# Kernel tuning notes

Measured on AMD Instinct MI355X. Metric: run time of the kernel, lower is better.

The kernel has to match this reference:

```python
import jax, jax.numpy as jnp
import numpy as np

N = 200000
E = 3200000
EPS = 1e-5


def setup_inputs() -> dict:
    key = jax.random.key(0)
    ks = jax.random.split(key, 8)
    x = jax.random.normal(ks[0], (N, 128), dtype=jnp.float32)
    edge_index = jax.random.randint(ks[1], (2, E), 0, N, dtype=jnp.int32)
    def lin(k, fi, fo):
        s = 1.0 / np.sqrt(fi)
        return jax.random.uniform(k, (fi, fo), jnp.float32, -s, s)
    return {
        "x": x,
        "edge_index": edge_index,
        "W1": lin(ks[2], 128, 256), "b1": jnp.zeros((256,), jnp.float32),
        "gamma1": jnp.ones((256,), jnp.float32), "beta1": jnp.zeros((256,), jnp.float32),
        "W2": lin(ks[3], 256, 256), "b2": jnp.zeros((256,), jnp.float32),
        "gamma2": jnp.ones((256,), jnp.float32), "beta2": jnp.zeros((256,), jnp.float32),
        "W3": lin(ks[4], 256, 40), "b3": jnp.zeros((40,), jnp.float32),
    }


def _gcn_norm(edge_index):
    # add self-loops, compute symmetric GCN normalization
    loop = jnp.arange(N, dtype=jnp.int32)
    row = jnp.concatenate([edge_index[0], loop])
    col = jnp.concatenate([edge_index[1], loop])
    deg = jax.ops.segment_sum(jnp.ones_like(row, dtype=jnp.float32), row, num_segments=N)
    dinv = jax.lax.rsqrt(jnp.maximum(deg, 1.0))  # deg >= 1 due to self-loops
    norm = dinv[row] * dinv[col]  # [E+N]
    return row, col, norm


def _gcn_conv(x, W, b, row, col, norm):
    h = x @ W                                  # [N, Fout] small GEMM
    msg = h[col] * norm[:, None]               # gather + scale  [E+N, Fout]
    out = jax.ops.segment_sum(msg, row, num_segments=N)  # scatter-add
    return out + b


def _batchnorm(x, gamma, beta):
    mu = jnp.mean(x, axis=0)
    var = jnp.var(x, axis=0)
    return (x - mu) * jax.lax.rsqrt(var + EPS) * gamma + beta


def reference(x, edge_index, W1, b1, gamma1, beta1, W2, b2, gamma2, beta2, W3, b3):
    row, col, norm = _gcn_norm(edge_index)
    h = _gcn_conv(x, W1, b1, row, col, norm)
    h = jax.nn.relu(_batchnorm(h, gamma1, beta1))
    h = _gcn_conv(h, W2, b2, row, col, norm)
    h = jax.nn.relu(_batchnorm(h, gamma2, beta2))
    h = _gcn_conv(h, W3, b3, row, col, norm)
    return jax.nn.log_softmax(h, axis=-1)
```

## Files before the change

kernel.cpp:

```cpp
#include <hip/hip_runtime.h>
#include <hip/hip_bf16.h>

#define NNODES 200000
#define NEDGES 3200000
#define NBUCK 782
#define NEB 512
#define EPB (NEDGES / NEB)
#define CASTB 12500
#define EPS 1e-5f

typedef __bf16 bf16x8 __attribute__((ext_vector_type(8)));
typedef float  f32x4  __attribute__((ext_vector_type(4)));
typedef float  f32x2  __attribute__((ext_vector_type(2)));

__device__ __forceinline__ float bflo(unsigned u) { return __uint_as_float(u << 16); }
__device__ __forceinline__ float bfhi(unsigned u) { return __uint_as_float(u & 0xffff0000u); }
__device__ __forceinline__ unsigned short f2b(float f) {
    return __builtin_bit_cast(unsigned short, __float2bfloat16(f));
}
__device__ __forceinline__ unsigned pk2(float a, float b) {
    return (unsigned)f2b(a) | ((unsigned)f2b(b) << 16);
}
__device__ __forceinline__ unsigned bnrelu_pk(unsigned u, f32x2 c, f32x2 h) {
    f32x2 v = { __uint_as_float(u << 16), __uint_as_float(u & 0xffff0000u) };
    v = __builtin_elementwise_fma(v, c, h);
    const f32x2 z = {0.f, 0.f};
    v = __builtin_elementwise_max(v, z);
    return pk2(v[0], v[1]);
}

__global__ __launch_bounds__(256) void k_cnt(const int* __restrict__ row, int* __restrict__ cnt) {
    __shared__ int h[NBUCK];
    for (int i = threadIdx.x; i < NBUCK; i += 256) h[i] = 0;
    __syncthreads();
    const int e0 = blockIdx.x * EPB;
    for (int i = e0 + threadIdx.x; i < e0 + EPB; i += 256)
        atomicAdd(&h[row[i] >> 8], 1);
    __syncthreads();
    for (int i = threadIdx.x; i < NBUCK; i += 256)
        cnt[(size_t)blockIdx.x * NBUCK + i] = h[i];
}

__global__ __launch_bounds__(256) void k_bscan(int* __restrict__ cnt, int* __restrict__ btot) {
    const int wv = (blockIdx.x * 256 + threadIdx.x) >> 6;
    const int lane = threadIdx.x & 63;
    if (wv >= NBUCK) return;
    int v[8]; int s = 0;
#pragma unroll
    for (int j = 0; j < 8; ++j) {
        v[j] = cnt[(size_t)(lane * 8 + j) * NBUCK + wv];
        s += v[j];
    }
    int excl = s;
#pragma unroll
    for (int o = 1; o < 64; o <<= 1) {
        int t = __shfl_up(excl, o);
        if (lane >= o) excl += t;
    }
    excl -= s;
    if (lane == 63) btot[wv] = excl + s;
    int base = excl;
#pragma unroll
    for (int j = 0; j < 8; ++j) {
        int t = v[j];
        cnt[(size_t)(lane * 8 + j) * NBUCK + wv] = base;
        base += t;
    }
}

__global__ __launch_bounds__(1024) void k_btscan(const int* __restrict__ btot, int* __restrict__ bbase) {
    __shared__ int s[1024];
    int t = threadIdx.x;
    int v = (t < NBUCK) ? btot[t] : 0;
    s[t] = v;
    __syncthreads();
    for (int off = 1; off < 1024; off <<= 1) {
        int u = (t >= off) ? s[t - off] : 0;
        __syncthreads();
        s[t] += u;
        __syncthreads();
    }
    if (t < NBUCK) bbase[t + 1] = s[t];
    if (t == 0) bbase[0] = 0;
}

__global__ __launch_bounds__(256) void k_place(const int* __restrict__ row, const int* __restrict__ col,
                                               const int* __restrict__ cnt, const int* __restrict__ bbase,
                                               unsigned* __restrict__ ebuf) {
    __shared__ int base[NBUCK];
    for (int i = threadIdx.x; i < NBUCK; i += 256)
        base[i] = bbase[i] + cnt[(size_t)blockIdx.x * NBUCK + i];
    __syncthreads();
    const int e0 = blockIdx.x * EPB;
    for (int i = e0 + threadIdx.x; i < e0 + EPB; i += 256) {
        int r = row[i], c = col[i];
        int p = atomicAdd(&base[r >> 8], 1);
        ebuf[p] = ((unsigned)(r & 255) << 18) | (unsigned)c;
    }
}

__global__ __launch_bounds__(256) void k_sort2(const unsigned* __restrict__ ebuf,
                                               const int* __restrict__ bbase,
                                               int* __restrict__ offs, float* __restrict__ dinv,
                                               int* __restrict__ csr) {
    __shared__ int cnt[256];
    __shared__ int sofs[256];
    __shared__ int sc[256];
    const int b = blockIdx.x;
    const int t = threadIdx.x;
    const int n0 = b * 256;
    cnt[t] = 0;
    __syncthreads();
    const int s = bbase[b], e = bbase[b + 1];
    for (int i = s + t; i < e; i += 256)
        atomicAdd(&cnt[ebuf[i] >> 18], 1);
    __syncthreads();
    const int c = cnt[t];
    sc[t] = c;
    __syncthreads();
    for (int off = 1; off < 256; off <<= 1) {
        int v = (t >= off) ? sc[t - off] : 0;
        __syncthreads();
        sc[t] += v;
        __syncthreads();
    }
    const int excl = sc[t] - c;
    sofs[t] = s + excl;
    const int n = n0 + t;
    if (n < NNODES) {
        offs[n] = s + excl;
        dinv[n] = rsqrtf((float)(c + 1));
    }
    if (b == NBUCK - 1 && t == 0) offs[NNODES] = NEDGES;
    cnt[t] = 0;
    __syncthreads();
    for (int i = s + t; i < e; i += 256) {
        unsigned v = ebuf[i];
        int nl = v >> 18;
        int rank = atomicAdd(&cnt[nl], 1);
        csr[sofs[nl] + rank] = (int)(v & 0x3FFFFu);
    }
}

__device__ __forceinline__ void prepw_one(const float* __restrict__ W,
                                          unsigned short* __restrict__ Wswz,
                                          int K, int NOUT, int t) {
    int KSTEPS = K / 32;
    int lane = t & 63;
    int ks = (t >> 6) % KSTEPS;
    int g  = (t >> 6) / KSTEPS;
    int c = lane & 15, q = lane >> 4;
    int col = g * 16 + c;
    int k0 = ks * 32 + q * 8;
    unsigned short vals[8];
#pragma unroll
    for (int j = 0; j < 8; ++j)
        vals[j] = (col < NOUT) ? f2b(W[(size_t)(k0 + j) * NOUT + col]) : (unsigned short)0;
    *(uint4*)((char*)Wswz + (size_t)t * 16) = __builtin_bit_cast(uint4, vals);
}

__global__ __launch_bounds__(256) void k_prep(const float* __restrict__ x,
                                              const float* __restrict__ dinv,
                                              uint4* __restrict__ xb,
                                              const float* __restrict__ W1,
                                              const float* __restrict__ W2,
                                              const float* __restrict__ W3,
                                              unsigned short* __restrict__ w1s,
                                              unsigned short* __restrict__ w2s,
                                              unsigned short* __restrict__ w3s) {
    const int blk = blockIdx.x;
    if (blk < CASTB) {
        size_t t = (size_t)blk * 256 + threadIdx.x;
        int n = (int)(t >> 4);
        float d = dinv[n];
        const float4* xp = (const float4*)(x + t * 8);
        float4 a = xp[0], b = xp[1];
        uint4 o;
        o.x = pk2(a.x * d, a.y * d); o.y = pk2(a.z * d, a.w * d);
        o.z = pk2(b.x * d, b.y * d); o.w = pk2(b.z * d, b.w * d);
        xb[t] = o;
    } else {
        int t = (blk - CASTB) * 256 + threadIdx.x;
        if (t < 4096) prepw_one(W1, w1s, 128, 256, t);
        else if (t < 4096 + 8192) prepw_one(W2, w2s, 256, 256, t - 4096);
        else if (t < 4096 + 8192 + 1536) prepw_one(W3, w3s, 256, 40, t - 12288);
    }
}

__global__ __launch_bounds__(256) void k_aggf(const uint4* __restrict__ in,
                                              const int* __restrict__ offs,
                                              const int* __restrict__ csr,
                                              const float* __restrict__ dinv,
                                              uint4* __restrict__ out) {
    const int lane = threadIdx.x & 63;
    const int grp = lane >> 4;
    const int fl = lane & 15;
    const int node = blockIdx.x * 4 + (threadIdx.x >> 6);
    const int p0 = offs[node];
    const int K = offs[node + 1] - p0 + 1;
    float a0=0,a1=0,a2=0,a3=0,a4=0,a5=0,a6=0,a7=0;
    auto accum = [&](uint4 u) {
        a0 += bflo(u.x); a1 += bfhi(u.x);
        a2 += bflo(u.y); a3 += bfhi(u.y);
        a4 += bflo(u.z); a5 += bfhi(u.z);
        a6 += bflo(u.w); a7 += bfhi(u.w);
    };
    int k = 0;
    for (; k + 16 <= K; k += 16) {
        int j0 = k + grp;
        int i0 = (j0 == 0) ? node : csr[p0 + j0 - 1];
        int i1 = csr[p0 + k + 3 + grp];
        int i2 = csr[p0 + k + 7 + grp];
        int i3 = csr[p0 + k + 11 + grp];
        uint4 u0 = in[(size_t)i0 * 16 + fl];
        uint4 u1 = in[(size_t)i1 * 16 + fl];
        uint4 u2 = in[(size_t)i2 * 16 + fl];
        uint4 u3 = in[(size_t)i3 * 16 + fl];
        accum(u0); accum(u1); accum(u2); accum(u3);
    }
    for (; k + 8 <= K; k += 8) {
        int j0 = k + grp;
        int i0 = (j0 == 0) ? node : csr[p0 + j0 - 1];
        int i1 = csr[p0 + k + 3 + grp];
        uint4 u0 = in[(size_t)i0 * 16 + fl];
        uint4 u1 = in[(size_t)i1 * 16 + fl];
        accum(u0); accum(u1);
    }
    for (; k + 4 <= K; k += 4) {
        int j0 = k + grp;
        int i0 = (j0 == 0) ? node : csr[p0 + j0 - 1];
        accum(in[(size_t)i0 * 16 + fl]);
    }
    int rem = K - k;
    if (grp < rem) {
        int j0 = k + grp;
        int i0 = (j0 == 0) ? node : csr[p0 + j0 - 1];
        accum(in[(size_t)i0 * 16 + fl]);
    }
#define RED(v) v += __shfl_xor(v, 32); v += __shfl_xor(v, 16);
    RED(a0) RED(a1) RED(a2) RED(a3) RED(a4) RED(a5) RED(a6) RED(a7)
#undef RED
    if (grp == 0) {
        const float d = dinv[node];
        uint4 o;
        o.x = pk2(a0 * d, a1 * d); o.y = pk2(a2 * d, a3 * d);
        o.z = pk2(a4 * d, a5 * d); o.w = pk2(a6 * d, a7 * d);
        out[(size_t)node * 16 + fl] = o;
    }
}

__global__ __launch_bounds__(256) void k_aggb(const uint4* __restrict__ in,
                                              const int* __restrict__ offs,
                                              const int* __restrict__ csr,
                                              const float* __restrict__ dinv,
                                              uint4* __restrict__ out) {
    const int lane = threadIdx.x & 63;
    const int half = lane >> 5;
    const int fl = lane & 31;
    const int node = blockIdx.x * 4 + (threadIdx.x >> 6);
    const int p0 = offs[node];
    const int K = offs[node + 1] - p0 + 1;
    float a0=0,a1=0,a2=0,a3=0,a4=0,a5=0,a6=0,a7=0;
    auto accum = [&](uint4 u) {
        a0 += bflo(u.x); a1 += bfhi(u.x);
        a2 += bflo(u.y); a3 += bfhi(u.y);
        a4 += bflo(u.z); a5 += bfhi(u.z);
        a6 += bflo(u.w); a7 += bfhi(u.w);
    };
    auto idxAt = [&](int j) -> int { return (j == 0) ? node : csr[p0 + j - 1]; };
    int k = 0;
    for (; k + 16 <= K; k += 16) {
        int i0 = idxAt(k + half);
        int i1 = csr[p0 + k + 1 + half];
        int i2 = csr[p0 + k + 3 + half];
        int i3 = csr[p0 + k + 5 + half];
        int i4 = csr[p0 + k + 7 + half];
        int i5 = csr[p0 + k + 9 + half];
        int i6 = csr[p0 + k + 11 + half];
        int i7 = csr[p0 + k + 13 + half];
        uint4 u0 = in[(size_t)i0 * 32 + fl];
        uint4 u1 = in[(size_t)i1 * 32 + fl];
        uint4 u2 = in[(size_t)i2 * 32 + fl];
        uint4 u3 = in[(size_t)i3 * 32 + fl];
        uint4 u4 = in[(size_t)i4 * 32 + fl];
        uint4 u5 = in[(size_t)i5 * 32 + fl];
        uint4 u6 = in[(size_t)i6 * 32 + fl];
        uint4 u7 = in[(size_t)i7 * 32 + fl];
        accum(u0); accum(u1); accum(u2); accum(u3);
        accum(u4); accum(u5); accum(u6); accum(u7);
    }
    for (; k + 8 <= K; k += 8) {
        int i0 = idxAt(k + half);
        int i1 = csr[p0 + k + 1 + half];
        int i2 = csr[p0 + k + 3 + half];
        int i3 = csr[p0 + k + 5 + half];
        uint4 u0 = in[(size_t)i0 * 32 + fl];
        uint4 u1 = in[(size_t)i1 * 32 + fl];
        uint4 u2 = in[(size_t)i2 * 32 + fl];
        uint4 u3 = in[(size_t)i3 * 32 + fl];
        accum(u0); accum(u1); accum(u2); accum(u3);
    }
    for (; k + 2 <= K; k += 2) {
        accum(in[(size_t)idxAt(k + half) * 32 + fl]);
    }
    if (k < K && half == 0) {
        accum(in[(size_t)idxAt(k) * 32 + fl]);
    }
#define RED(v) v += __shfl_xor(v, 32);
    RED(a0) RED(a1) RED(a2) RED(a3) RED(a4) RED(a5) RED(a6) RED(a7)
#undef RED
    if (half == 0) {
        const float d = dinv[node];
        uint4 o;
        o.x = pk2(a0 * d, a1 * d); o.y = pk2(a2 * d, a3 * d);
        o.z = pk2(a4 * d, a5 * d); o.w = pk2(a6 * d, a7 * d);
        out[(size_t)node * 32 + fl] = o;
    }
}

__global__ __launch_bounds__(256) void k_agg3(const uint4* __restrict__ T3b,
                                              const int* __restrict__ offs,
                                              const int* __restrict__ csr,
                                              const float* __restrict__ dinv,
                                              const float* __restrict__ b3,
                                              float* __restrict__ out) {
    const int lane = threadIdx.x & 63;
    const int grp = lane / 5;
    const int fl = lane - grp * 5;
    const bool act = grp < 12;
    const int node = blockIdx.x * 4 + (threadIdx.x >> 6);
    const int p0 = offs[node];
    const int K = offs[node + 1] - p0 + 1;
    float a0=0,a1=0,a2=0,a3=0,a4=0,a5=0,a6=0,a7=0;
    auto accum = [&](uint4 u) {
        a0 += bflo(u.x); a1 += bfhi(u.x);
        a2 += bflo(u.y); a3 += bfhi(u.y);
        a4 += bflo(u.z); a5 += bfhi(u.z);
        a6 += bflo(u.w); a7 += bfhi(u.w);
    };
    const char* Tb = (const char*)T3b;
    int k = 0;
    if (act) {
        for (; k + 12 <= K; k += 12) {
            int j = k + grp;
            int i0 = (j == 0) ? node : csr[p0 + j - 1];
            accum(*(const uint4*)(Tb + (size_t)i0 * 128 + fl * 16));
        }
        int rem = K - k;
        if (grp < rem) {
            int j = k + grp;
            int i0 = (j == 0) ? node : csr[p0 + j - 1];
            accum(*(const uint4*)(Tb + (size_t)i0 * 128 + fl * 16));
        }
    }
#define RED3(v) { float t = __shfl(v, lane + 30); v += t; t = __shfl(v, lane + 15); v += t; \
                  float u1 = __shfl(v, lane + 5); float u2 = __shfl(v, lane + 10); v += u1 + u2; }
    RED3(a0) RED3(a1) RED3(a2) RED3(a3) RED3(a4) RED3(a5) RED3(a6) RED3(a7)
#undef RED3
    const float d = dinv[node];
    float v[8];
    if (grp == 0) {
        const float4* bp = (const float4*)(b3 + fl * 8);
        float4 b01 = bp[0], b23 = bp[1];
        v[0] = a0 * d + b01.x; v[1] = a1 * d + b01.y;
        v[2] = a2 * d + b01.z; v[3] = a3 * d + b01.w;
        v[4] = a4 * d + b23.x; v[5] = a5 * d + b23.y;
        v[6] = a6 * d + b23.z; v[7] = a7 * d + b23.w;
    } else {
#pragma unroll
        for (int j = 0; j < 8; ++j) v[j] = -INFINITY;
    }
    float m = v[0];
#pragma unroll
    for (int j = 1; j < 8; ++j) m = fmaxf(m, v[j]);
    float mm = __shfl(m, 0);
#pragma unroll
    for (int l = 1; l < 5; ++l) mm = fmaxf(mm, __shfl(m, l));
    float e = 0.f;
    if (grp == 0) {
#pragma unroll
        for (int j = 0; j < 8; ++j) e += __expf(v[j] - mm);
    }
    float s = __shfl(e, 0);
#pragma unroll
    for (int l = 1; l < 5; ++l) s += __shfl(e, l);
    float ls = __logf(s);
    if (grp == 0) {
        float* op = out + (size_t)node * 40 + fl * 8;
        float4 o0 = {v[0] - mm - ls, v[1] - mm - ls, v[2] - mm - ls, v[3] - mm - ls};
        float4 o1 = {v[4] - mm - ls, v[5] - mm - ls, v[6] - mm - ls, v[7] - mm - ls};
        *(float4*)op = o0;
        *(float4*)(op + 4) = o1;
    }
}

template <int K, int MW, int NW, int WNB, bool PRESCALE, bool BNA, bool STATS>
__global__ __launch_bounds__(MW * NW * 64) void k_gemm(const __hip_bfloat16* __restrict__ A,
                                                       const __hip_bfloat16* __restrict__ Wswz,
                                                       const float* __restrict__ dinvp,
                                                       const float* __restrict__ bnsc,
                                                       const float* __restrict__ bnsh,
                                                       unsigned short* __restrict__ Cout,
                                                       int M, int NOUT, int CS,
                                                       float* __restrict__ sums,
                                                       float* __restrict__ sq) {
    constexpr int KSTEPS = K / 32;
    const int lane = threadIdx.x & 63;
    const int wid  = threadIdx.x >> 6;
    const int wm = (wid % MW) * 64;
    const int wn = (wid / MW) * (WNB * 16);
    const long rowBase = (long)blockIdx.x * (MW * 64);
    const int cl = lane & 15, q = lane >> 4;

    const __hip_bfloat16* aptr[4];
#pragma unroll
    for (int mf = 0; mf < 4; ++mf) {
        long r = rowBase + wm + mf * 16 + cl;
        if (r > M - 1) r = M - 1;
        aptr[mf] = A + r * K + q * 8;
    }
    const __hip_bfloat16* bptr[WNB];
#pragma unroll
    for (int nf = 0; nf < WNB; ++nf) {
        int g = wn / 16 + nf;
        bptr[nf] = Wswz + (size_t)g * KSTEPS * 512 + (size_t)lane * 8;
    }

    f32x4 acc[4][WNB];
    const f32x4 z = {0.f, 0.f, 0.f, 0.f};
#pragma unroll
    for (int mf = 0; mf < 4; ++mf)
#pragma unroll
        for (int nf = 0; nf < WNB; ++nf) acc[mf][nf] = z;

#pragma unroll
    for (int ks = 0; ks < KSTEPS; ++ks) {
        f32x2 cp0, cp1, cp2, cp3, hp0, hp1, hp2, hp3;
        if constexpr (BNA) {
            const int k0 = ks * 32 + q * 8;
            const f32x2* cp = (const f32x2*)(bnsc + k0);
            const f32x2* hp = (const f32x2*)(bnsh + k0);
            cp0 = cp[0]; cp1 = cp[1]; cp2 = cp[2]; cp3 = cp[3];
            hp0 = hp[0]; hp1 = hp[1]; hp2 = hp[2]; hp3 = hp[3];
        }
        bf16x8 a[4], b[WNB];
#pragma unroll
        for (int mf = 0; mf < 4; ++mf) {
            uint4 u = *(const uint4*)(aptr[mf] + ks * 32);
            if constexpr (BNA) {
                uint4 o;
                o.x = bnrelu_pk(u.x, cp0, hp0);
                o.y = bnrelu_pk(u.y, cp1, hp1);
                o.z = bnrelu_pk(u.z, cp2, hp2);
                o.w = bnrelu_pk(u.w, cp3, hp3);
                u = o;
            }
            a[mf] = __builtin_bit_cast(bf16x8, u);
        }
#pragma unroll
        for (int nf = 0; nf < WNB; ++nf)
            b[nf] = __builtin_bit_cast(bf16x8, *(const uint4*)(bptr[nf] + ks * 512));
#pragma unroll
        for (int mf = 0; mf < 4; ++mf)
#pragma unroll
            for (int nf = 0; nf < WNB; ++nf)
                acc[mf][nf] = __builtin_amdgcn_mfma_f32_16x16x32_bf16(a[mf], b[nf], acc[mf][nf], 0, 0, 0);
    }

#pragma unroll
    for (int mf = 0; mf < 4; ++mf)
#pragma unroll
        for (int i = 0; i < 4; ++i) {
            long row = rowBase + wm + mf * 16 + q * 4 + i;
            if (row >= M) continue;
            float dv = PRESCALE ? dinvp[row] : 1.0f;
#pragma unroll
            for (int nf = 0; nf < WNB; ++nf) {
                int col = wn + nf * 16 + cl;
                if (col < NOUT)
                    Cout[row * CS + col] = f2b(PRESCALE ? acc[mf][nf][i] * dv : acc[mf][nf][i]);
            }
        }

    if constexpr (STATS) {
#pragma unroll
        for (int nf = 0; nf < WNB; ++nf) {
            float s = 0.f, s2 = 0.f;
#pragma unroll
            for (int mf = 0; mf < 4; ++mf)
#pragma unroll
                for (int i = 0; i < 4; ++i) {
                    long row = rowBase + wm + mf * 16 + q * 4 + i;
                    float v = (row < M) ? acc[mf][nf][i] : 0.f;
                    s += v; s2 += v * v;
                }
            s  += __shfl_xor(s, 16);  s  += __shfl_xor(s, 32);
            s2 += __shfl_xor(s2, 16); s2 += __shfl_xor(s2, 32);
            if (q == 0) {
                int col = wn + nf * 16 + cl;
                if (col < NOUT) {
                    atomicAdd(&sums[col], s);
                    atomicAdd(&sq[col], s2);
                }
            }
        }
    }
}

__global__ __launch_bounds__(256) void k_bnfin(const float* __restrict__ sums,
                                               const float* __restrict__ sq,
                                               const float* __restrict__ gamma,
                                               const float* __restrict__ beta,
                                               float* __restrict__ scale,
                                               float* __restrict__ shift) {
    const int t = threadIdx.x;
    float mu = sums[t] * (1.0f / NNODES);
    float var = sq[t] * (1.0f / NNODES) - mu * mu;
    if (var < 0.f) var = 0.f;
    float sc = gamma[t] * rsqrtf(var + EPS);
    scale[t] = sc;
    shift[t] = beta[t] - mu * sc;
}

__global__ __launch_bounds__(256) void k_stats(const uint4* __restrict__ Zu,
                                               float* __restrict__ sums, float* __restrict__ sq) {
    __shared__ float reds[8][256];
    __shared__ float redq[8][256];
    const int t = threadIdx.x;
    const int cg = t & 31;
    const int rs = t >> 5;
    const long r0 = (long)blockIdx.x * 256 + (long)rs * 32;
    float s[8], q[8];
#pragma unroll
    for (int j = 0; j < 8; ++j) { s[j] = 0.f; q[j] = 0.f; }
    for (int i = 0; i < 32; ++i) {
        long r = r0 + i;
        if (r >= NNODES) break;
        uint4 u = Zu[r * 32 + cg];
        float v0 = bflo(u.x), v1 = bfhi(u.x), v2 = bflo(u.y), v3 = bfhi(u.y);
        float v4 = bflo(u.z), v5 = bfhi(u.z), v6 = bflo(u.w), v7 = bfhi(u.w);
        s[0] += v0; q[0] += v0 * v0;  s[1] += v1; q[1] += v1 * v1;
        s[2] += v2; q[2] += v2 * v2;  s[3] += v3; q[3] += v3 * v3;
        s[4] += v4; q[4] += v4 * v4;  s[5] += v5; q[5] += v5 * v5;
        s[6] += v6; q[6] += v6 * v6;  s[7] += v7; q[7] += v7 * v7;
    }
#pragma unroll
    for (int j = 0; j < 8; ++j) {
        reds[rs][cg * 8 + j] = s[j];
        redq[rs][cg * 8 + j] = q[j];
    }
    __syncthreads();
    float S = 0.f, Q = 0.f;
#pragma unroll
    for (int j = 0; j < 8; ++j) { S += reds[j][t]; Q += redq[j][t]; }
    atomicAdd(&sums[t], S);
    atomicAdd(&sq[t], Q);
}

extern "C" void kernel_launch(void* const* d_in, const int* in_sizes, int n_in,
                              void* d_out, int out_size, void* d_ws, size_t ws_size,
                              hipStream_t stream) {
    const float* x   = (const float*)d_in[0];
    const int*   ei  = (const int*)d_in[1];
    const float* W1  = (const float*)d_in[2];
    const float* g1  = (const float*)d_in[4];
    const float* be1 = (const float*)d_in[5];
    const float* W2  = (const float*)d_in[6];
    const float* g2  = (const float*)d_in[8];
    const float* be2 = (const float*)d_in[9];
    const float* W3  = (const float*)d_in[10];
    const float* b3  = (const float*)d_in[11];

    char* w = (char*)d_ws;
    size_t o = 0;
    auto alloc = [&](size_t b) { size_t r = o; o += (b + 255) & ~(size_t)255; return r; };
    int*   offs = (int*)(w + alloc((size_t)(NNODES + 1) * 4));
    float* dinv = (float*)(w + alloc((size_t)NNODES * 4));
    int*   cnt  = (int*)(w + alloc((size_t)NEB * NBUCK * 4));
    int*   btot = (int*)(w + alloc(NBUCK * 4));
    int*   bbase= (int*)(w + alloc((NBUCK + 1) * 4));
    unsigned* ebuf = (unsigned*)(w + alloc((size_t)NEDGES * 4));
    int*   csr  = (int*)(w + alloc((size_t)NEDGES * 4));
    float* stats = (float*)(w + alloc(4 * 256 * 4 + 32));
    float* bnp   = (float*)(w + alloc(4 * 256 * 4));
    unsigned short* w1s = (unsigned short*)(w + alloc(65536));
    unsigned short* w2s = (unsigned short*)(w + alloc(131072));
    unsigned short* w3s = (unsigned short*)(w + alloc(24576));
    __hip_bfloat16* xb   = (__hip_bfloat16*)(w + alloc((size_t)NNODES * 128 * 2));
    __hip_bfloat16* buf0 = (__hip_bfloat16*)(w + alloc((size_t)NNODES * 128 * 2));
    __hip_bfloat16* buf1 = (__hip_bfloat16*)(w + alloc((size_t)NNODES * 256 * 2));
    __hip_bfloat16* buf2 = (__hip_bfloat16*)(w + alloc((size_t)NNODES * 256 * 2));

    float* sums1 = stats;       float* sq1 = stats + 256;
    float* sums2 = stats + 512; float* sq2 = stats + 768;
    float* scale1 = bnp;        float* shift1 = bnp + 256;
    float* scale2 = bnp + 512;  float* shift2 = bnp + 768;

    hipMemsetAsync(stats, 0, 4 * 256 * 4 + 32, stream);

    const int SB = (NNODES + 255) / 256;
    k_cnt<<<NEB, 256, 0, stream>>>(ei, cnt);
    k_bscan<<<(NBUCK * 64 + 255) / 256, 256, 0, stream>>>(cnt, btot);
    k_btscan<<<1, 1024, 0, stream>>>(btot, bbase);
    k_place<<<NEB, 256, 0, stream>>>(ei, ei + NEDGES, cnt, bbase, ebuf);
    k_sort2<<<NBUCK, 256, 0, stream>>>(ebuf, bbase, offs, dinv, csr);
    k_prep<<<CASTB + 54, 256, 0, stream>>>(x, dinv, (uint4*)xb, W1, W2, W3, w1s, w2s, w3s);

    const dim3 g64((NNODES + 63) / 64, 1);

    k_aggf<<<NNODES / 4, 256, 0, stream>>>((const uint4*)xb, offs, csr, dinv, (uint4*)buf0);
    k_gemm<128, 1, 4, 4, false, false, true><<<g64, 256, 0, stream>>>(buf0, (const __hip_bfloat16*)w1s, nullptr, nullptr, nullptr, (unsigned short*)buf1, NNODES, 256, 256, sums1, sq1);
    k_bnfin<<<1, 256, 0, stream>>>(sums1, sq1, g1, be1, scale1, shift1);

    k_gemm<256, 1, 4, 4, true, true, false><<<g64, 256, 0, stream>>>(buf1, (const __hip_bfloat16*)w2s, dinv, scale1, shift1, (unsigned short*)buf2, NNODES, 256, 256, nullptr, nullptr);
    k_aggb<<<NNODES / 4, 256, 0, stream>>>((const uint4*)buf2, offs, csr, dinv, (uint4*)buf1);
    k_stats<<<SB, 256, 0, stream>>>((const uint4*)buf1, sums2, sq2);
    k_bnfin<<<1, 256, 0, stream>>>(sums2, sq2, g2, be2, scale2, shift2);

    k_gemm<256, 4, 1, 3, true, true, false><<<dim3((NNODES + 255) / 256, 1), 256, 0, stream>>>(buf1, (const __hip_bfloat16*)w3s, dinv, scale2, shift2, (unsigned short*)buf0, NNODES, 40, 64, nullptr, nullptr);
    k_agg3<<<NNODES / 4, 256, 0, stream>>>((const uint4*)buf0, offs, csr, dinv, b3, (float*)d_out);
}
```

Baseline: 1.070 ms.

## Fuse preprocessing and BN-finalize kernels to cut launch count

Folds the weight swizzle and stats zeroing into the bucket-count kernel, merges the bucket-total scan into each placement block, and moves the x-to-bf16 scaling cast into the CSR sort kernel. BatchNorm finalization now runs in the last block of the GEMM and stats kernels, detected with an atomic done counter. The 16-wide unroll in the feature aggregation loop is also removed. This removes several small launches and the memset, at the cost of redundant scans in every placement block and a last-block reduction pattern that depends on correct memory ordering.

Result: no change. 1.076 ms (+0.5%).

```diff
diff --git a/kernel.cpp b/kernel.cpp
--- a/kernel.cpp
+++ b/kernel.cpp
@@ -6,7 +6,6 @@
 #define NBUCK 782
 #define NEB 512
 #define EPB (NEDGES / NEB)
-#define CASTB 12500
 #define EPS 1e-5f
 
 typedef __bf16 bf16x8 __attribute__((ext_vector_type(8)));
@@ -27,119 +26,6 @@
     const f32x2 z = {0.f, 0.f};
     v = __builtin_elementwise_max(v, z);
     return pk2(v[0], v[1]);
-}
-
-__global__ __launch_bounds__(256) void k_cnt(const int* __restrict__ row, int* __restrict__ cnt) {
-    __shared__ int h[NBUCK];
-    for (int i = threadIdx.x; i < NBUCK; i += 256) h[i] = 0;
-    __syncthreads();
-    const int e0 = blockIdx.x * EPB;
-    for (int i = e0 + threadIdx.x; i < e0 + EPB; i += 256)
-        atomicAdd(&h[row[i] >> 8], 1);
-    __syncthreads();
-    for (int i = threadIdx.x; i < NBUCK; i += 256)
-        cnt[(size_t)blockIdx.x * NBUCK + i] = h[i];
-}
-
-__global__ __launch_bounds__(256) void k_bscan(int* __restrict__ cnt, int* __restrict__ btot) {
-    const int wv = (blockIdx.x * 256 + threadIdx.x) >> 6;
-    const int lane = threadIdx.x & 63;
-    if (wv >= NBUCK) return;
-    int v[8]; int s = 0;
-#pragma unroll
-    for (int j = 0; j < 8; ++j) {
-        v[j] = cnt[(size_t)(lane * 8 + j) * NBUCK + wv];
-        s += v[j];
-    }
-    int excl = s;
-#pragma unroll
-    for (int o = 1; o < 64; o <<= 1) {
-        int t = __shfl_up(excl, o);
-        if (lane >= o) excl += t;
-    }
-    excl -= s;
-    if (lane == 63) btot[wv] = excl + s;
-    int base = excl;
-#pragma unroll
-    for (int j = 0; j < 8; ++j) {
-        int t = v[j];
-        cnt[(size_t)(lane * 8 + j) * NBUCK + wv] = base;
-        base += t;
-    }
-}
-
-__global__ __launch_bounds__(1024) void k_btscan(const int* __restrict__ btot, int* __restrict__ bbase) {
-    __shared__ int s[1024];
-    int t = threadIdx.x;
-    int v = (t < NBUCK) ? btot[t] : 0;
-    s[t] = v;
-    __syncthreads();
-    for (int off = 1; off < 1024; off <<= 1) {
-        int u = (t >= off) ? s[t - off] : 0;
-        __syncthreads();
-        s[t] += u;
-        __syncthreads();
-    }
-    if (t < NBUCK) bbase[t + 1] = s[t];
-    if (t == 0) bbase[0] = 0;
-}
-
-__global__ __launch_bounds__(256) void k_place(const int* __restrict__ row, const int* __restrict__ col,
-                                               const int* __restrict__ cnt, const int* __restrict__ bbase,
-                                               unsigned* __restrict__ ebuf) {
-    __shared__ int base[NBUCK];
-    for (int i = threadIdx.x; i < NBUCK; i += 256)
-        base[i] = bbase[i] + cnt[(size_t)blockIdx.x * NBUCK + i];
-    __syncthreads();
-    const int e0 = blockIdx.x * EPB;
-    for (int i = e0 + threadIdx.x; i < e0 + EPB; i += 256) {
-        int r = row[i], c = col[i];
-        int p = atomicAdd(&base[r >> 8], 1);
-        ebuf[p] = ((unsigned)(r & 255) << 18) | (unsigned)c;
-    }
-}
-
-__global__ __launch_bounds__(256) void k_sort2(const unsigned* __restrict__ ebuf,
-                                               const int* __restrict__ bbase,
-                                               int* __restrict__ offs, float* __restrict__ dinv,
-                                               int* __restrict__ csr) {
-    __shared__ int cnt[256];
-    __shared__ int sofs[256];
-    __shared__ int sc[256];
-    const int b = blockIdx.x;
-    const int t = threadIdx.x;
-    const int n0 = b * 256;
-    cnt[t] = 0;
-    __syncthreads();
-    const int s = bbase[b], e = bbase[b + 1];
-    for (int i = s + t; i < e; i += 256)
-        atomicAdd(&cnt[ebuf[i] >> 18], 1);
-    __syncthreads();
-    const int c = cnt[t];
-    sc[t] = c;
-    __syncthreads();
-    for (int off = 1; off < 256; off <<= 1) {
-        int v = (t >= off) ? sc[t - off] : 0;
-        __syncthreads();
-        sc[t] += v;
-        __syncthreads();
-    }
-    const int excl = sc[t] - c;
-    sofs[t] = s + excl;
-    const int n = n0 + t;
-    if (n < NNODES) {
-        offs[n] = s + excl;
-        dinv[n] = rsqrtf((float)(c + 1));
-    }
-    if (b == NBUCK - 1 && t == 0) offs[NNODES] = NEDGES;
-    cnt[t] = 0;
-    __syncthreads();
-    for (int i = s + t; i < e; i += 256) {
-        unsigned v = ebuf[i];
-        int nl = v >> 18;
-        int rank = atomicAdd(&cnt[nl], 1);
-        csr[sofs[nl] + rank] = (int)(v & 0x3FFFFu);
-    }
 }
 
 __device__ __forceinline__ void prepw_one(const float* __restrict__ W,
@@ -159,31 +45,167 @@
     *(uint4*)((char*)Wswz + (size_t)t * 16) = __builtin_bit_cast(uint4, vals);
 }
 
-__global__ __launch_bounds__(256) void k_prep(const float* __restrict__ x,
-                                              const float* __restrict__ dinv,
-                                              uint4* __restrict__ xb,
-                                              const float* __restrict__ W1,
-                                              const float* __restrict__ W2,
-                                              const float* __restrict__ W3,
-                                              unsigned short* __restrict__ w1s,
-                                              unsigned short* __restrict__ w2s,
-                                              unsigned short* __restrict__ w3s) {
+__global__ __launch_bounds__(256) void k_cnt(const int* __restrict__ row, int* __restrict__ cnt,
+                                             const float* __restrict__ W1,
+                                             const float* __restrict__ W2,
+                                             const float* __restrict__ W3,
+                                             unsigned short* __restrict__ w1s,
+                                             unsigned short* __restrict__ w2s,
+                                             unsigned short* __restrict__ w3s,
+                                             unsigned* __restrict__ statsz) {
     const int blk = blockIdx.x;
-    if (blk < CASTB) {
-        size_t t = (size_t)blk * 256 + threadIdx.x;
-        int n = (int)(t >> 4);
-        float d = dinv[n];
-        const float4* xp = (const float4*)(x + t * 8);
-        float4 a = xp[0], b = xp[1];
+    if (blk == NEB + 54) {
+        for (int i = threadIdx.x; i < 1026; i += 256) statsz[i] = 0u;
+        return;
+    }
+    if (blk >= NEB) {
+        int t = (blk - NEB) * 256 + threadIdx.x;
+        if (t < 4096) prepw_one(W1, w1s, 128, 256, t);
+        else if (t < 12288) prepw_one(W2, w2s, 256, 256, t - 4096);
+        else if (t < 13824) prepw_one(W3, w3s, 256, 40, t - 12288);
+        return;
+    }
+    __shared__ int h[NBUCK];
+    for (int i = threadIdx.x; i < NBUCK; i += 256) h[i] = 0;
+    __syncthreads();
+    const int e0 = blk * EPB;
+    for (int i = e0 + threadIdx.x; i < e0 + EPB; i += 256)
+        atomicAdd(&h[row[i] >> 8], 1);
+    __syncthreads();
+    for (int i = threadIdx.x; i < NBUCK; i += 256)
+        cnt[(size_t)blk * NBUCK + i] = h[i];
+}
+
+__global__ __launch_bounds__(256) void k_bscan(int* __restrict__ cnt, int* __restrict__ btot) {
+    const int wv = (blockIdx.x * 256 + threadIdx.x) >> 6;
+    const int lane = threadIdx.x & 63;
+    if (wv >= NBUCK) return;
+    int v[8]; int s = 0;
+#pragma unroll
+    for (int j = 0; j < 8; ++j) {
+        v[j] = cnt[(size_t)(lane * 8 + j) * NBUCK + wv];
+        s += v[j];
+    }
+    int excl = s;
+#pragma unroll
+    for (int o = 1; o < 64; o <<= 1) {
+        int t = __shfl_up(excl, o);
+        if (lane >= o) excl += t;
+    }
+    excl -= s;
+    if (lane == 63) btot[wv] = excl + s;
+    int base = excl;
+#pragma unroll
+    for (int j = 0; j < 8; ++j) {
+        int t = v[j];
+        cnt[(size_t)(lane * 8 + j) * NBUCK + wv] = base;
+        base += t;
+    }
+}
+
+__global__ __launch_bounds__(256) void k_place(const int* __restrict__ row, const int* __restrict__ col,
+                                               const int* __restrict__ cnt, const int* __restrict__ btot,
+                                               int* __restrict__ bbase, unsigned* __restrict__ ebuf) {
+    __shared__ int sbb[NBUCK];
+    __shared__ int tp[256];
+    __shared__ int base[NBUCK];
+    const int t = threadIdx.x;
+    int v[4]; int loc = 0;
+    const int i0 = t * 4;
+#pragma unroll
+    for (int j = 0; j < 4; ++j) {
+        int idx = i0 + j;
+        v[j] = (idx < NBUCK) ? btot[idx] : 0;
+        loc += v[j];
+    }
+    tp[t] = loc;
+    __syncthreads();
+    for (int off = 1; off < 256; off <<= 1) {
+        int u = (t >= off) ? tp[t - off] : 0;
+        __syncthreads();
+        tp[t] += u;
+        __syncthreads();
+    }
+    int run = tp[t] - loc;
+#pragma unroll
+    for (int j = 0; j < 4; ++j) {
+        int idx = i0 + j;
+        if (idx < NBUCK) sbb[idx] = run;
+        run += v[j];
+    }
+    __syncthreads();
+    if (blockIdx.x == 0) {
+        for (int i = t; i < NBUCK; i += 256) bbase[i] = sbb[i];
+        if (t == 0) bbase[NBUCK] = NEDGES;
+    }
+    for (int i = t; i < NBUCK; i += 256)
+        base[i] = sbb[i] + cnt[(size_t)blockIdx.x * NBUCK + i];
+    __syncthreads();
+    const int e0 = blockIdx.x * EPB;
+    for (int i = e0 + t; i < e0 + EPB; i += 256) {
+        int r = row[i], c = col[i];
+        int p = atomicAdd(&base[r >> 8], 1);
+        ebuf[p] = ((unsigned)(r & 255) << 18) | (unsigned)c;
+    }
+}
+
+__global__ __launch_bounds__(256) void k_sort2(const unsigned* __restrict__ ebuf,
+                                               const int* __restrict__ bbase,
+                                               int* __restrict__ offs, float* __restrict__ dinv,
+                                               int* __restrict__ csr,
+                                               const float* __restrict__ x,
+                                               uint4* __restrict__ xb) {
+    __shared__ int cnt[256];
+    __shared__ int sofs[256];
+    __shared__ int sc[256];
+    __shared__ float sdinv[256];
+    const int b = blockIdx.x;
+    const int t = threadIdx.x;
+    const int n0 = b * 256;
+    cnt[t] = 0;
+    __syncthreads();
+    const int s = bbase[b], e = bbase[b + 1];
+    for (int i = s + t; i < e; i += 256)
+        atomicAdd(&cnt[ebuf[i] >> 18], 1);
+    __syncthreads();
+    const int c = cnt[t];
+    sc[t] = c;
+    __syncthreads();
+    for (int off = 1; off < 256; off <<= 1) {
+        int v = (t >= off) ? sc[t - off] : 0;
+        __syncthreads();
+        sc[t] += v;
+        __syncthreads();
+    }
+    const int excl = sc[t] - c;
+    sofs[t] = s + excl;
+    const int n = n0 + t;
+    float dv = rsqrtf((float)(c + 1));
+    sdinv[t] = dv;
+    if (n < NNODES) {
+        offs[n] = s + excl;
+        dinv[n] = dv;
+    }
+    if (b == NBUCK - 1 && t == 0) offs[NNODES] = NEDGES;
+    cnt[t] = 0;
+    __syncthreads();
+    for (int i = s + t; i < e; i += 256) {
+        unsigned v = ebuf[i];
+        int nl = v >> 18;
+        int rank = atomicAdd(&cnt[nl], 1);
+        csr[sofs[nl] + rank] = (int)(v & 0x3FFFFu);
+    }
+    const int nn = (NNODES - n0 < 256) ? (NNODES - n0) : 256;
+    const float4* xp = (const float4*)(x + (size_t)n0 * 128);
+    uint4* xo = xb + (size_t)n0 * 16;
+    const int lim = nn * 16;
+    for (int i = t; i < lim; i += 256) {
+        float d = sdinv[i >> 4];
+        float4 a = xp[i * 2], bb = xp[i * 2 + 1];
         uint4 o;
-        o.x = pk2(a.x * d, a.y * d); o.y = pk2(a.z * d, a.w * d);
-        o.z = pk2(b.x * d, b.y * d); o.w = pk2(b.z * d, b.w * d);
-        xb[t] = o;
-    } else {
-        int t = (blk - CASTB) * 256 + threadIdx.x;
-        if (t < 4096) prepw_one(W1, w1s, 128, 256, t);
-        else if (t < 4096 + 8192) prepw_one(W2, w2s, 256, 256, t - 4096);
-        else if (t < 4096 + 8192 + 1536) prepw_one(W3, w3s, 256, 40, t - 12288);
+        o.x = pk2(a.x * d, a.y * d);  o.y = pk2(a.z * d, a.w * d);
+        o.z = pk2(bb.x * d, bb.y * d); o.w = pk2(bb.z * d, bb.w * d);
+        xo[i] = o;
     }
 }
 
@@ -269,26 +291,6 @@
     };
     auto idxAt = [&](int j) -> int { return (j == 0) ? node : csr[p0 + j - 1]; };
     int k = 0;
-    for (; k + 16 <= K; k += 16) {
-        int i0 = idxAt(k + half);
-        int i1 = csr[p0 + k + 1 + half];
-        int i2 = csr[p0 + k + 3 + half];
-        int i3 = csr[p0 + k + 5 + half];
-        int i4 = csr[p0 + k + 7 + half];
-        int i5 = csr[p0 + k + 9 + half];
-        int i6 = csr[p0 + k + 11 + half];
-        int i7 = csr[p0 + k + 13 + half];
-        uint4 u0 = in[(size_t)i0 * 32 + fl];
-        uint4 u1 = in[(size_t)i1 * 32 + fl];
-        uint4 u2 = in[(size_t)i2 * 32 + fl];
-        uint4 u3 = in[(size_t)i3 * 32 + fl];
-        uint4 u4 = in[(size_t)i4 * 32 + fl];
-        uint4 u5 = in[(size_t)i5 * 32 + fl];
-        uint4 u6 = in[(size_t)i6 * 32 + fl];
-        uint4 u7 = in[(size_t)i7 * 32 + fl];
-        accum(u0); accum(u1); accum(u2); accum(u3);
-        accum(u4); accum(u5); accum(u6); accum(u7);
-    }
     for (; k + 8 <= K; k += 8) {
         int i0 = idxAt(k + half);
         int i1 = csr[p0 + k + 1 + half];
@@ -403,7 +405,12 @@
                                                        unsigned short* __restrict__ Cout,
                                                        int M, int NOUT, int CS,
                                                        float* __restrict__ sums,
-                                                       float* __restrict__ sq) {
+                                                       float* __restrict__ sq,
+                                                       const float* __restrict__ gamma,
+                                                       const float* __restrict__ beta,
+                                                       float* __restrict__ scale,
+                                                       float* __restrict__ shift,
+                                                       int* __restrict__ done) {
     constexpr int KSTEPS = K / 32;
     const int lane = threadIdx.x & 63;
     const int wid  = threadIdx.x >> 6;
@@ -504,26 +511,30 @@
                 }
             }
         }
-    }
-}
-
-__global__ __launch_bounds__(256) void k_bnfin(const float* __restrict__ sums,
-                                               const float* __restrict__ sq,
+        __syncthreads();
+        __shared__ int lastf;
+        if (threadIdx.x == 0) lastf = (atomicAdd(done, 1) == (int)gridDim.x - 1) ? 1 : 0;
+        __syncthreads();
+        if (lastf) {
+            const int tt = threadIdx.x;
+            float su = atomicAdd(&sums[tt], 0.0f);
+            float qu = atomicAdd(&sq[tt], 0.0f);
+            float mu = su * (1.0f / NNODES);
+            float var = qu * (1.0f / NNODES) - mu * mu;
+            if (var < 0.f) var = 0.f;
+            float sc = gamma[tt] * rsqrtf(var + EPS);
+            scale[tt] = sc;
+            shift[tt] = beta[tt] - mu * sc;
+        }
+    }
+}
+
+__global__ __launch_bounds__(256) void k_stats(const uint4* __restrict__ Zu,
+                                               float* __restrict__ sums, float* __restrict__ sq,
                                                const float* __restrict__ gamma,
                                                const float* __restrict__ beta,
-                                               float* __restrict__ scale,
-                                               float* __restrict__ shift) {
-    const int t = threadIdx.x;
-    float mu = sums[t] * (1.0f / NNODES);
-    float var = sq[t] * (1.0f / NNODES) - mu * mu;
-    if (var < 0.f) var = 0.f;
-    float sc = gamma[t] * rsqrtf(var + EPS);
-    scale[t] = sc;
-    shift[t] = beta[t] - mu * sc;
-}
-
-__global__ __launch_bounds__(256) void k_stats(const uint4* __restrict__ Zu,
-                                               float* __restrict__ sums, float* __restrict__ sq) {
+                                               float* __restrict__ scale, float* __restrict__ shift,
+                                               int* __restrict__ done) {
     __shared__ float reds[8][256];
     __shared__ float redq[8][256];
     const int t = threadIdx.x;
@@ -555,6 +566,20 @@
     for (int j = 0; j < 8; ++j) { S += reds[j][t]; Q += redq[j][t]; }
     atomicAdd(&sums[t], S);
     atomicAdd(&sq[t], Q);
+    __syncthreads();
+    __shared__ int lastf;
+    if (t == 0) lastf = (atomicAdd(done, 1) == (int)gridDim.x - 1) ? 1 : 0;
+    __syncthreads();
+    if (lastf) {
+        float su = atomicAdd(&sums[t], 0.0f);
+        float qu = atomicAdd(&sq[t], 0.0f);
+        float mu = su * (1.0f / NNODES);
+        float var = qu * (1.0f / NNODES) - mu * mu;
+        if (var < 0.f) var = 0.f;
+        float sc = gamma[t] * rsqrtf(var + EPS);
+        scale[t] = sc;
+        shift[t] = beta[t] - mu * sc;
+    }
 }
 
 extern "C" void kernel_launch(void* const* d_in, const int* in_sizes, int n_in,
@@ -593,30 +618,27 @@
 
     float* sums1 = stats;       float* sq1 = stats + 256;
     float* sums2 = stats + 512; float* sq2 = stats + 768;
+    int*   done1 = (int*)(stats + 1024);
+    int*   done2 = done1 + 1;
     float* scale1 = bnp;        float* shift1 = bnp + 256;
     float* scale2 = bnp + 512;  float* shift2 = bnp + 768;
 
-    hipMemsetAsync(stats, 0, 4 * 256 * 4 + 32, stream);
-
     const int SB = (NNODES + 255) / 256;
-    k_cnt<<<NEB, 256, 0, stream>>>(ei, cnt);
+
+    k_cnt<<<NEB + 55, 256, 0, stream>>>(ei, cnt, W1, W2, W3, w1s, w2s, w3s, (unsigned*)stats);
     k_bscan<<<(NBUCK * 64 + 255) / 256, 256, 0, stream>>>(cnt, btot);
-    k_btscan<<<1, 1024, 0, stream>>>(btot, bbase);
-    k_place<<<NEB, 256, 0, stream>>>(ei, ei + NEDGES, cnt, bbase, ebuf);
-    k_sort2<<<NBUCK, 256, 0, stream>>>(ebuf, bbase, offs, dinv, csr);
-    k_prep<<<CASTB + 54, 256, 0, stream>>>(x, dinv, (uint4*)xb, W1, W2, W3, w1s, w2s, w3s);
+    k_place<<<NEB, 256, 0, stream>>>(ei, ei + NEDGES, cnt, btot, bbase, ebuf);
+    k_sort2<<<NBUCK, 256, 0, stream>>>(ebuf, bbase, offs, dinv, csr, x, (uint4*)xb);
 
     const dim3 g64((NNODES + 63) / 64, 1);
 
     k_aggf<<<NNODES / 4, 256, 0, stream>>>((const uint4*)xb, offs, csr, dinv, (uint4*)buf0);
-    k_gemm<128, 1, 4, 4, false, false, true><<<g64, 256, 0, stream>>>(buf0, (const __hip_bfloat16*)w1s, nullptr, nullptr, nullptr, (unsigned short*)buf1, NNODES, 256, 256, sums1, sq1);
-    k_bnfin<<<1, 256, 0, stream>>>(sums1, sq1, g1, be1, scale1, shift1);
-
-    k_gemm<256, 1, 4, 4, true, true, false><<<g64, 256, 0, stream>>>(buf1, (const __hip_bfloat16*)w2s, dinv, scale1, shift1, (unsigned short*)buf2, NNODES, 256, 256, nullptr, nullptr);
+    k_gemm<128, 1, 4, 4, false, false, true><<<g64, 256, 0, stream>>>(buf0, (const __hip_bfloat16*)w1s, nullptr, nullptr, nullptr, (unsigned short*)buf1, NNODES, 256, 256, sums1, sq1, g1, be1, scale1, shift1, done1);
+
+    k_gemm<256, 1, 4, 4, true, true, false><<<g64, 256, 0, stream>>>(buf1, (const __hip_bfloat16*)w2s, dinv, scale1, shift1, (unsigned short*)buf2, NNODES, 256, 256, nullptr, nullptr, nullptr, nullptr, nullptr, nullptr, nullptr);
     k_aggb<<<NNODES / 4, 256, 0, stream>>>((const uint4*)buf2, offs, csr, dinv, (uint4*)buf1);
-    k_stats<<<SB, 256, 0, stream>>>((const uint4*)buf1, sums2, sq2);
-    k_bnfin<<<1, 256, 0, stream>>>(sums2, sq2, g2, be2, scale2, shift2);
-
-    k_gemm<256, 4, 1, 3, true, true, false><<<dim3((NNODES + 255) / 256, 1), 256, 0, stream>>>(buf1, (const __hip_bfloat16*)w3s, dinv, scale2, shift2, (unsigned short*)buf0, NNODES, 40, 64, nullptr, nullptr);
+    k_stats<<<SB, 256, 0, stream>>>((const uint4*)buf1, sums2, sq2, g2, be2, scale2, shift2, done2);
+
+    k_gemm<256, 4, 1, 3, true, true, false><<<dim3((NNODES + 255) / 256, 1), 256, 0, stream>>>(buf1, (const __hip_bfloat16*)w3s, dinv, scale2, shift2, (unsigned short*)buf0, NNODES, 40, 64, nullptr, nullptr, nullptr, nullptr, nullptr, nullptr, nullptr);
     k_agg3<<<NNODES / 4, 256, 0, stream>>>((const uint4*)buf0, offs, csr, dinv, b3, (float*)d_out);
 }
```
